# Kernel optimization log

Hardware: AMD Instinct MI355X
Metric: run time of the kernel (lower is better)

## Reference

```python
import jax, jax.numpy as jnp
import numpy as np

HIDDEN = 896
N_HEADS = 14
N_KV_HEADS = 2
HEAD_DIM = HIDDEN // N_HEADS  # 64
KV_GROUPS = N_HEADS // N_KV_HEADS  # 7
ROPE_THETA = 1000000.0


def rotate_half(x):
    x1, x2 = x[..., : x.shape[-1] // 2], x[..., x.shape[-1] // 2 :]
    return jnp.concatenate((-x2, x1), axis=-1)


def rope_tables(seq_len, dtype=jnp.float32):
    inv_freq = 1.0 / (ROPE_THETA ** (jnp.arange(0, HEAD_DIM, 2, dtype=jnp.float32) / HEAD_DIM))
    t = jnp.arange(seq_len, dtype=jnp.float32)
    freqs = jnp.outer(t, inv_freq)            # [S, D/2]
    emb = jnp.concatenate((freqs, freqs), -1)  # [S, D]
    return jnp.cos(emb).astype(dtype), jnp.sin(emb).astype(dtype)


def setup_inputs() -> dict:
    key = jax.random.key(0)
    ks = jax.random.split(key, 8)
    B, S = 2, 2048
    s = 0.02
    return {
        "hidden_states": jax.random.normal(ks[0], (B, S, HIDDEN), jnp.float32),
        "wq": jax.random.normal(ks[1], (HIDDEN, N_HEADS * HEAD_DIM), jnp.float32) * s,
        "bq": jnp.zeros((N_HEADS * HEAD_DIM,), jnp.float32),
        "wk": jax.random.normal(ks[2], (HIDDEN, N_KV_HEADS * HEAD_DIM), jnp.float32) * s,
        "bk": jnp.zeros((N_KV_HEADS * HEAD_DIM,), jnp.float32),
        "wv": jax.random.normal(ks[3], (HIDDEN, N_KV_HEADS * HEAD_DIM), jnp.float32) * s,
        "bv": jnp.zeros((N_KV_HEADS * HEAD_DIM,), jnp.float32),
        "wo": jax.random.normal(ks[4], (N_HEADS * HEAD_DIM, HIDDEN), jnp.float32) * s,
    }


def reference(hidden_states, wq, bq, wk, bk, wv, bv, wo):
    B, S, _ = hidden_states.shape
    q = (hidden_states @ wq + bq).reshape(B, S, N_HEADS, HEAD_DIM)
    k = (hidden_states @ wk + bk).reshape(B, S, N_KV_HEADS, HEAD_DIM)
    v = (hidden_states @ wv + bv).reshape(B, S, N_KV_HEADS, HEAD_DIM)

    cos, sin = rope_tables(S, hidden_states.dtype)
    cos, sin = cos[None, :, None, :], sin[None, :, None, :]
    q = q * cos + rotate_half(q) * sin
    k = k * cos + rotate_half(k) * sin

    # GQA broadcast: repeat kv heads to match query heads
    k = jnp.repeat(k, KV_GROUPS, axis=2)
    v = jnp.repeat(v, KV_GROUPS, axis=2)

    # [B, H, S, S]
    scores = jnp.einsum("bqhd,bkhd->bhqk", q, k) / jnp.sqrt(jnp.asarray(HEAD_DIM, hidden_states.dtype))
    mask = jnp.tril(jnp.ones((S, S), dtype=jnp.bool_))
    scores = jnp.where(mask[None, None, :, :], scores, jnp.asarray(-1e9, scores.dtype))
    attn = jax.nn.softmax(scores, axis=-1)
    out = jnp.einsum("bhqk,bkhd->bqhd", attn, v).reshape(B, S, N_HEADS * HEAD_DIM)
    return out @ wo
```

## Files before the change

### kernel.cpp

```cpp
#include <hip/hip_runtime.h>

#define HID 896
#define NQ 896
#define NKV 128
#define NQKV 1152
#define NH 14
#define NKVH 2
#define GQ 7
#define DH 64
#define SEQ 2048
#define BATCH 2
#define TOK (BATCH*SEQ)

typedef __attribute__((ext_vector_type(8))) short short8;
typedef __attribute__((ext_vector_type(4))) float f32x4;
typedef __attribute__((ext_vector_type(4))) unsigned short us4;

__device__ __forceinline__ unsigned short f2bf(float x) {
  unsigned int u = __builtin_bit_cast(unsigned int, x);
  u = (u + 0x7fffu + ((u >> 16) & 1u)) >> 16;
  return (unsigned short)u;
}
__device__ __forceinline__ float bf2f(unsigned short b) {
  return __builtin_bit_cast(float, (unsigned int)b << 16);
}
__device__ __forceinline__ f32x4 fzero4() {
  f32x4 z; z[0]=0.f; z[1]=0.f; z[2]=0.f; z[3]=0.f; return z;
}
__device__ __forceinline__ unsigned int cvt_pk_bf16(float lo, float hi) {
  unsigned int r;
  asm("v_cvt_pk_bf16_f32 %0, %1, %2" : "=v"(r) : "v"(lo), "v"(hi));
  return r;
}
__device__ __forceinline__ void gload_lds16(const unsigned short* g, unsigned short* l) {
  __builtin_amdgcn_global_load_lds(
      (const __attribute__((address_space(1))) void*)(const void*)g,
      (__attribute__((address_space(3))) void*)(void*)l, 16, 0, 0);
}

#define CVT_BLKS 3584
#define TRN_BLKS 448
#define BIAS_BLKS 5
#define TAB_BLKS 256
#define PREP_BLKS (CVT_BLKS + TRN_BLKS + BIAS_BLKS + TAB_BLKS)

__global__ void k_prep(const float* __restrict__ hs,
                       const float* __restrict__ wq, const float* __restrict__ bq,
                       const float* __restrict__ wk, const float* __restrict__ bk,
                       const float* __restrict__ wv, const float* __restrict__ bv,
                       const float* __restrict__ wo,
                       unsigned short* __restrict__ hb,
                       unsigned short* __restrict__ wqkvt,
                       unsigned short* __restrict__ wot,
                       float* __restrict__ bqkv,
                       float* __restrict__ ct, float* __restrict__ st) {
  __shared__ unsigned short Ls[64*65];
  int blk = blockIdx.x, tid = threadIdx.x;
  if (blk < CVT_BLKS) {
    int i = blk*256 + tid;
    float4 v = ((const float4*)hs)[i];
    us4 o; o[0]=f2bf(v.x); o[1]=f2bf(v.y); o[2]=f2bf(v.z); o[3]=f2bf(v.w);
    ((us4*)hb)[i] = o;
    return;
  }
  blk -= CVT_BLKS;
  if (blk < TRN_BLKS) {
    const float* W; unsigned short* out; int K, N, n0, k0;
    if (blk < 196)      { W=wq; out=wqkvt;                        K=HID; N=NQ;  int t=blk;     n0=(t%14)*64; k0=(t/14)*64; }
    else if (blk < 224) { W=wk; out=wqkvt + (size_t)NQ*HID;       K=HID; N=NKV; int t=blk-196; n0=(t%2)*64;  k0=(t/2)*64; }
    else if (blk < 252) { W=wv; out=wqkvt + (size_t)(NQ+NKV)*HID; K=HID; N=NKV; int t=blk-224; n0=(t%2)*64;  k0=(t/2)*64; }
    else                { W=wo; out=wot;                          K=NQ;  N=HID; int t=blk-252; n0=(t%14)*64; k0=(t/14)*64; }
    #pragma unroll
    for (int i = 0; i < 16; ++i) {
      int idx = i*256 + tid;
      int r = idx >> 6, c = idx & 63;
      Ls[c*65 + r] = f2bf(W[(size_t)(k0 + r)*N + n0 + c]);
    }
    __syncthreads();
    #pragma unroll
    for (int i = 0; i < 16; ++i) {
      int idx = i*256 + tid;
      int r2 = idx >> 6, c2 = idx & 63;
      out[(size_t)(n0 + r2)*K + k0 + c2] = Ls[r2*65 + c2];
    }
    return;
  }
  blk -= TRN_BLKS;
  if (blk < BIAS_BLKS) {
    int i = blk*256 + tid;
    if (i < NQKV) {
      if (i < NQ) bqkv[i] = bq[i];
      else if (i < NQ + NKV) bqkv[i] = bk[i - NQ];
      else bqkv[i] = bv[i - NQ - NKV];
    }
    return;
  }
  blk -= BIAS_BLKS;
  {
    int i = blk*256 + tid;
    int s = i >> 5, dp = i & 31;
    float inv = __expf(-(float)(2*dp) * (13.815510557964274f / 64.0f));
    float f = (float)s * inv;
    ct[i] = cosf(f); st[i] = sinf(f);
  }
}

template<int OUTMODE>
__global__ __launch_bounds__(256, 2) void k_gemm_bt(
    const unsigned short* __restrict__ A,
    const unsigned short* __restrict__ Bt,
    const float* __restrict__ bias,
    void* __restrict__ Cout,
    int M, int N, int K) {
  __shared__ unsigned short As[128*64];
  __shared__ unsigned short Bs[128*64];
  int tid = threadIdx.x;
  int lane = tid & 63, w = tid >> 6;
  int wr = w >> 1, wc = w & 1;
  int l15 = lane & 15, l4 = lane >> 4;
  int m0 = blockIdx.y * 128, n0 = blockIdx.x * 128;

  f32x4 acc[4][4];
  #pragma unroll
  for (int i = 0; i < 4; ++i)
    #pragma unroll
    for (int j = 0; j < 4; ++j) acc[i][j] = fzero4();

  int nkt = K >> 6;
  for (int kt = 0; kt < nkt; ++kt) {
    int k0 = kt << 6;
    #pragma unroll
    for (int t = 0; t < 4; ++t) {
      int chunk = t*256 + w*64 + lane;
      int row = chunk >> 3, sp = chunk & 7;
      int sl = sp ^ (row & 7);
      gload_lds16(A + (size_t)(m0+row)*K + k0 + sl*8, &As[(t*256 + w*64)*8]);
      gload_lds16(Bt + (size_t)(n0+row)*K + k0 + sl*8, &Bs[(t*256 + w*64)*8]);
    }
    __syncthreads();
    #pragma unroll
    for (int s = 0; s < 2; ++s) {
      short8 af[4], bfr[4];
      #pragma unroll
      for (int mi = 0; mi < 4; ++mi) {
        int row = wr*64 + mi*16 + l15;
        int slot = (s*4 + l4) ^ (row & 7);
        af[mi] = *reinterpret_cast<const short8*>(&As[row*64 + slot*8]);
      }
      #pragma unroll
      for (int ni = 0; ni < 4; ++ni) {
        int row = wc*64 + ni*16 + l15;
        int slot = (s*4 + l4) ^ (row & 7);
        bfr[ni] = *reinterpret_cast<const short8*>(&Bs[row*64 + slot*8]);
      }
      #pragma unroll
      for (int mi = 0; mi < 4; ++mi)
        #pragma unroll
        for (int ni = 0; ni < 4; ++ni)
          acc[mi][ni] = __builtin_amdgcn_mfma_f32_16x16x32_bf16(af[mi], bfr[ni], acc[mi][ni], 0, 0, 0);
    }
    __syncthreads();
  }
  #pragma unroll
  for (int mi = 0; mi < 4; ++mi) {
    #pragma unroll
    for (int ni = 0; ni < 4; ++ni) {
      #pragma unroll
      for (int r = 0; r < 4; ++r) {
        int row = m0 + wr*64 + mi*16 + l4*4 + r;
        int col = n0 + wc*64 + ni*16 + l15;
        float v = acc[mi][ni][r];
        if (OUTMODE == 0) {
          v += bias[col];
          ((unsigned short*)Cout)[(size_t)row*N + col] = f2bf(v);
        } else {
          ((float*)Cout)[(size_t)row*N + col] = v;
        }
      }
    }
  }
}

__global__ void k_rope(const unsigned short* __restrict__ qkv,
                       const float* __restrict__ ct, const float* __restrict__ st,
                       unsigned short* __restrict__ Qr, unsigned short* __restrict__ Kr,
                       unsigned short* __restrict__ Vt) {
  int t = blockIdx.x; int b = t >> 11; int s = t & 2047;
  int tid = threadIdx.x;
  const unsigned short* row = qkv + (size_t)t * NQKV;
  if (tid < 448) {
    int h = tid >> 5, dp = tid & 31;
    float x1 = bf2f(row[h*64 + dp]);
    float x2 = bf2f(row[h*64 + dp + 32]);
    float c = ct[s*32 + dp], sn = st[s*32 + dp];
    size_t base = (((size_t)b*NH + h)*SEQ + s)*64;
    Qr[base + dp]      = f2bf((x1*c - x2*sn) * 0.125f);
    Qr[base + dp + 32] = f2bf((x2*c + x1*sn) * 0.125f);
  } else {
    int j = tid - 448;
    int kvh = j >> 5, dp = j & 31;
    float x1 = bf2f(row[NQ + kvh*64 + dp]);
    float x2 = bf2f(row[NQ + kvh*64 + dp + 32]);
    float c = ct[s*32 + dp], sn = st[s*32 + dp];
    size_t base = (((size_t)b*NKVH + kvh)*SEQ + s)*64;
    Kr[base + dp]      = f2bf(x1*c - x2*sn);
    Kr[base + dp + 32] = f2bf(x2*c + x1*sn);
  }
  if (tid < 128) {
    int kvh = tid >> 6, d = tid & 63;
    Vt[(((size_t)b*NKVH + kvh)*64 + d)*SEQ + s] = row[1024 + kvh*64 + d];
  }
}

__global__ __launch_bounds__(256, 2) void k_attn(
    const unsigned short* __restrict__ Q,
    const unsigned short* __restrict__ Kr,
    const unsigned short* __restrict__ Vt,
    unsigned short* __restrict__ Aout) {
  __shared__ __align__(16) unsigned short Kst[2][64*64];
  __shared__ __align__(16) unsigned short Vst[2][64*64];
  __shared__ __align__(16) unsigned short P_lds[2][4*16*64];
  int lane = threadIdx.x & 63, w = threadIdx.x >> 6;
  int l15 = lane & 15, l4 = lane >> 4;
  int i = blockIdx.x, h = blockIdx.y, b = blockIdx.z;
  int qtH = 31 - i, qtL = i;
  int kvh = h / GQ;
  const unsigned short* Kb = Kr + ((size_t)(b*NKVH + kvh))*SEQ*64;
  const unsigned short* Vb = Vt + ((size_t)(b*NKVH + kvh))*64*SEQ;
  char* PwH = (char*)&P_lds[0][w*16*64];
  char* PwL = (char*)&P_lds[1][w*16*64];

  auto stage = [&](int kt, int bsel) {
    #pragma unroll
    for (int t = 0; t < 2; ++t) {
      int chunk = t*256 + w*64 + lane;
      int row = chunk >> 3;
      int sl = (chunk & 7) ^ (row & 7);
      gload_lds16(Kb + (size_t)(kt*64 + row)*64 + sl*8, &Kst[bsel][(t*256 + w*64)*8]);
      gload_lds16(Vb + (size_t)row*SEQ + kt*64 + sl*8, &Vst[bsel][(t*256 + w*64)*8]);
    }
  };

  const unsigned short* QbH = Q + (((size_t)(b*NH + h))*SEQ + qtH*64 + w*16) * 64;
  const unsigned short* QbL = Q + (((size_t)(b*NH + h))*SEQ + qtL*64 + w*16) * 64;
  short8 qaH[2], qaL[2];
  #pragma unroll
  for (int s = 0; s < 2; ++s) {
    qaH[s] = *reinterpret_cast<const short8*>(QbH + l15*64 + s*32 + l4*8);
    qaL[s] = *reinterpret_cast<const short8*>(QbL + l15*64 + s*32 + l4*8);
  }

  f32x4 accH[4], accL[4];
  #pragma unroll
  for (int n = 0; n < 4; ++n) { accH[n] = fzero4(); accL[n] = fzero4(); }
  float mH = -__builtin_inff(), lH = 0.0f;
  float mL = -__builtin_inff(), lL = 0.0f;

  int cur = 0;

  auto tile = [&](int kt, bool diag, short8 (&qa)[2], f32x4 (&acc)[4],
                  float& m_run, float& l_run, int qt, char* Pwb) {
    f32x4 sa[4];
    #pragma unroll
    for (int n = 0; n < 4; ++n) sa[n] = fzero4();
    #pragma unroll
    for (int s = 0; s < 2; ++s) {
      short8 kb[4];
      #pragma unroll
      for (int n = 0; n < 4; ++n) {
        int row = n*16 + l15;
        int slot = (s*4 + l4) ^ (row & 7);
        kb[n] = *reinterpret_cast<const short8*>(&Kst[cur][row*64 + slot*8]);
      }
      #pragma unroll
      for (int n = 0; n < 4; ++n)
        sa[n] = __builtin_amdgcn_mfma_f32_16x16x32_bf16(kb[n], qa[s], sa[n], 0, 0, 0);
    }
    if (diag) {
      int q_glob = qt*64 + w*16 + l15;
      #pragma unroll
      for (int n = 0; n < 4; ++n)
        #pragma unroll
        for (int r = 0; r < 4; ++r) {
          int kpos = kt*64 + n*16 + l4*4 + r;
          if (kpos > q_glob) sa[n][r] = -1e30f;
        }
    }
    float t01 = fmaxf(fmaxf(sa[0][0],sa[0][1]), fmaxf(sa[0][2],sa[0][3]));
    float t11 = fmaxf(fmaxf(sa[1][0],sa[1][1]), fmaxf(sa[1][2],sa[1][3]));
    float t21 = fmaxf(fmaxf(sa[2][0],sa[2][1]), fmaxf(sa[2][2],sa[2][3]));
    float t31 = fmaxf(fmaxf(sa[3][0],sa[3][1]), fmaxf(sa[3][2],sa[3][3]));
    float tmax = fmaxf(fmaxf(t01,t11), fmaxf(t21,t31));
    tmax = fmaxf(tmax, __shfl_xor(tmax, 16));
    tmax = fmaxf(tmax, __shfl_xor(tmax, 32));
    float mn = fmaxf(m_run, tmax);
    float sc = __expf(m_run - mn);
    #pragma unroll
    for (int n = 0; n < 4; ++n)
      #pragma unroll
      for (int r = 0; r < 4; ++r) sa[n][r] = __expf(sa[n][r] - mn);
    float s0 = (sa[0][0]+sa[0][1]) + (sa[0][2]+sa[0][3]);
    float s1 = (sa[1][0]+sa[1][1]) + (sa[1][2]+sa[1][3]);
    float s2r = (sa[2][0]+sa[2][1]) + (sa[2][2]+sa[2][3]);
    float s3 = (sa[3][0]+sa[3][1]) + (sa[3][2]+sa[3][3]);
    float sum = (s0+s1) + (s2r+s3);
    sum += __shfl_xor(sum, 16);
    sum += __shfl_xor(sum, 32);
    m_run = mn;
    l_run = l_run*sc + sum;
    #pragma unroll
    for (int n = 0; n < 4; ++n) acc[n] *= sc;
    #pragma unroll
    for (int n = 0; n < 4; ++n) {
      uint2 pk;
      pk.x = cvt_pk_bf16(sa[n][0], sa[n][1]);
      pk.y = cvt_pk_bf16(sa[n][2], sa[n][3]);
      int colbyte = n*32 + l4*8;
      int addr = l15*128 + ((((colbyte>>4) ^ (l15&7))) << 4) + (colbyte & 15);
      *reinterpret_cast<uint2*>(Pwb + addr) = pk;
    }
    #pragma unroll
    for (int s2 = 0; s2 < 2; ++s2) {
      int pslot = (s2*4 + l4) ^ (l15 & 7);
      short8 pa = *reinterpret_cast<const short8*>(Pwb + l15*128 + pslot*16);
      #pragma unroll
      for (int n = 0; n < 4; ++n) {
        int row = n*16 + l15;
        int vslot = (s2*4 + l4) ^ (row & 7);
        short8 vb = *reinterpret_cast<const short8*>(&Vst[cur][row*64 + vslot*8]);
        acc[n] = __builtin_amdgcn_mfma_f32_16x16x32_bf16(vb, pa, acc[n], 0, 0, 0);
      }
    }
  };

  stage(0, 0);
  __syncthreads();
  int nkt = qtH + 1;
  for (int kt = 0; kt < nkt; ++kt) {
    if (kt + 1 < nkt) stage(kt + 1, cur ^ 1);
    tile(kt, kt == qtH, qaH, accH, mH, lH, qtH, PwH);
    if (kt <= qtL) tile(kt, kt == qtL, qaL, accL, mL, lL, qtL, PwL);
    __syncthreads();
    cur ^= 1;
  }

  auto epi = [&](f32x4 (&acc)[4], float l_run, int qt, char* Pwb) {
    float inv = 1.0f / l_run;
    #pragma unroll
    for (int n = 0; n < 4; ++n) {
      uint2 pk;
      pk.x = cvt_pk_bf16(acc[n][0]*inv, acc[n][1]*inv);
      pk.y = cvt_pk_bf16(acc[n][2]*inv, acc[n][3]*inv);
      int colbyte = n*32 + l4*8;
      int addr = l15*128 + ((((colbyte>>4) ^ (l15&7))) << 4) + (colbyte & 15);
      *reinterpret_cast<uint2*>(Pwb + addr) = pk;
    }
    int row = lane >> 2;
    int cb0 = (lane & 3) * 32;
    #pragma unroll
    for (int it = 0; it < 2; ++it) {
      int cb = cb0 + it*16;
      int slot = (cb >> 4) ^ (row & 7);
      short8 v = *reinterpret_cast<const short8*>(Pwb + row*128 + slot*16);
      size_t tok = (size_t)b*SEQ + qt*64 + w*16 + row;
      *reinterpret_cast<short8*>(&Aout[tok*NQ + h*64 + (cb>>1)]) = v;
    }
  };
  epi(accH, lH, qtH, PwH);
  epi(accL, lL, qtL, PwL);
}

extern "C" void kernel_launch(void* const* d_in, const int* in_sizes, int n_in,
                              void* d_out, int out_size, void* d_ws, size_t ws_size,
                              hipStream_t stream) {
  const float* hs = (const float*)d_in[0];
  const float* wq = (const float*)d_in[1];
  const float* bq = (const float*)d_in[2];
  const float* wk = (const float*)d_in[3];
  const float* bk = (const float*)d_in[4];
  const float* wv = (const float*)d_in[5];
  const float* bv = (const float*)d_in[6];
  const float* wo = (const float*)d_in[7];
  float* out = (float*)d_out;

  char* p = (char*)d_ws;
  auto alloc = [&](size_t bytes) { char* r = p; p += (bytes + 255) & ~(size_t)255; return r; };
  unsigned short* hb    = (unsigned short*)alloc((size_t)TOK*HID*2);
  unsigned short* wqkvt = (unsigned short*)alloc((size_t)NQKV*HID*2);
  unsigned short* wot   = (unsigned short*)alloc((size_t)HID*NQ*2);
  float*          bqkv  = (float*)alloc(NQKV*4);
  unsigned short* qkvt  = (unsigned short*)alloc((size_t)TOK*NQKV*2);
  unsigned short* q_r   = (unsigned short*)alloc((size_t)BATCH*NH*SEQ*DH*2);
  unsigned short* k_r   = (unsigned short*)alloc((size_t)BATCH*NKVH*SEQ*DH*2);
  unsigned short* v_t   = (unsigned short*)alloc((size_t)BATCH*NKVH*DH*SEQ*2);
  float*          ct    = (float*)alloc((size_t)SEQ*32*4);
  float*          st    = (float*)alloc((size_t)SEQ*32*4);
  unsigned short* attn  = hb;

  k_prep<<<PREP_BLKS, 256, 0, stream>>>(hs, wq, bq, wk, bk, wv, bv, wo,
                                        hb, wqkvt, wot, bqkv, ct, st);
  k_gemm_bt<0><<<dim3(NQKV/128, TOK/128), 256, 0, stream>>>(hb, wqkvt, bqkv, qkvt, TOK, NQKV, HID);
  k_rope<<<TOK, 512, 0, stream>>>(qkvt, ct, st, q_r, k_r, v_t);
  k_attn<<<dim3(16, NH, BATCH), 256, 0, stream>>>(q_r, k_r, v_t, attn);
  k_gemm_bt<1><<<dim3(NQ/128, TOK/128), 256, 0, stream>>>(attn, wot, nullptr, out, TOK, NQ, HID);
}
```

Before: 104.1 us.

## Drop LDS K/V staging in attention, load directly from global, one q-tile per block

The attention kernel no longer stages K and V tiles into double-buffered shared memory with barriers. Each wave now reads its K and V fragments straight from global memory (relying on cache), and the paired high/low q-tile scheme is replaced by one q-tile per block with a doubled grid. Occupancy is raised to 3 blocks per CU because shared memory use shrinks to the P buffer. This removes the per-tile __syncthreads and LDS staging cost, but every wave now issues its own K/V global loads with no cross-wave reuse, and causal load balancing now depends on reversed block ordering.

Result: slower. 285.6 us (+174.4%).

```diff
diff --git a/kernel.cpp b/kernel.cpp
--- a/kernel.cpp
+++ b/kernel.cpp
@@ -212,54 +212,33 @@
   }
 }
 
-__global__ __launch_bounds__(256, 2) void k_attn(
+__global__ __launch_bounds__(256, 3) void k_attn(
     const unsigned short* __restrict__ Q,
     const unsigned short* __restrict__ Kr,
     const unsigned short* __restrict__ Vt,
     unsigned short* __restrict__ Aout) {
-  __shared__ __align__(16) unsigned short Kst[2][64*64];
-  __shared__ __align__(16) unsigned short Vst[2][64*64];
-  __shared__ __align__(16) unsigned short P_lds[2][4*16*64];
+  __shared__ __align__(16) unsigned short P_lds[4][16*64];
   int lane = threadIdx.x & 63, w = threadIdx.x >> 6;
   int l15 = lane & 15, l4 = lane >> 4;
-  int i = blockIdx.x, h = blockIdx.y, b = blockIdx.z;
-  int qtH = 31 - i, qtL = i;
+  int qt = (int)gridDim.x - 1 - (int)blockIdx.x;
+  int h = blockIdx.y, b = blockIdx.z;
   int kvh = h / GQ;
   const unsigned short* Kb = Kr + ((size_t)(b*NKVH + kvh))*SEQ*64;
   const unsigned short* Vb = Vt + ((size_t)(b*NKVH + kvh))*64*SEQ;
-  char* PwH = (char*)&P_lds[0][w*16*64];
-  char* PwL = (char*)&P_lds[1][w*16*64];
-
-  auto stage = [&](int kt, int bsel) {
-    #pragma unroll
-    for (int t = 0; t < 2; ++t) {
-      int chunk = t*256 + w*64 + lane;
-      int row = chunk >> 3;
-      int sl = (chunk & 7) ^ (row & 7);
-      gload_lds16(Kb + (size_t)(kt*64 + row)*64 + sl*8, &Kst[bsel][(t*256 + w*64)*8]);
-      gload_lds16(Vb + (size_t)row*SEQ + kt*64 + sl*8, &Vst[bsel][(t*256 + w*64)*8]);
-    }
-  };
-
-  const unsigned short* QbH = Q + (((size_t)(b*NH + h))*SEQ + qtH*64 + w*16) * 64;
-  const unsigned short* QbL = Q + (((size_t)(b*NH + h))*SEQ + qtL*64 + w*16) * 64;
-  short8 qaH[2], qaL[2];
-  #pragma unroll
-  for (int s = 0; s < 2; ++s) {
-    qaH[s] = *reinterpret_cast<const short8*>(QbH + l15*64 + s*32 + l4*8);
-    qaL[s] = *reinterpret_cast<const short8*>(QbL + l15*64 + s*32 + l4*8);
-  }
-
-  f32x4 accH[4], accL[4];
-  #pragma unroll
-  for (int n = 0; n < 4; ++n) { accH[n] = fzero4(); accL[n] = fzero4(); }
-  float mH = -__builtin_inff(), lH = 0.0f;
-  float mL = -__builtin_inff(), lL = 0.0f;
-
-  int cur = 0;
-
-  auto tile = [&](int kt, bool diag, short8 (&qa)[2], f32x4 (&acc)[4],
-                  float& m_run, float& l_run, int qt, char* Pwb) {
+  char* Pw = (char*)&P_lds[w][0];
+
+  const unsigned short* Qb = Q + (((size_t)(b*NH + h))*SEQ + qt*64 + w*16) * 64;
+  short8 qa[2];
+  #pragma unroll
+  for (int s = 0; s < 2; ++s)
+    qa[s] = *reinterpret_cast<const short8*>(Qb + l15*64 + s*32 + l4*8);
+
+  f32x4 acc[4];
+  #pragma unroll
+  for (int n = 0; n < 4; ++n) acc[n] = fzero4();
+  float m_run = -__builtin_inff(), l_run = 0.0f;
+
+  for (int kt = 0; kt <= qt; ++kt) {
     f32x4 sa[4];
     #pragma unroll
     for (int n = 0; n < 4; ++n) sa[n] = fzero4();
@@ -267,16 +246,21 @@
     for (int s = 0; s < 2; ++s) {
       short8 kb[4];
       #pragma unroll
-      for (int n = 0; n < 4; ++n) {
-        int row = n*16 + l15;
-        int slot = (s*4 + l4) ^ (row & 7);
-        kb[n] = *reinterpret_cast<const short8*>(&Kst[cur][row*64 + slot*8]);
-      }
+      for (int n = 0; n < 4; ++n)
+        kb[n] = *reinterpret_cast<const short8*>(
+            Kb + (size_t)(kt*64 + n*16 + l15)*64 + s*32 + l4*8);
       #pragma unroll
       for (int n = 0; n < 4; ++n)
         sa[n] = __builtin_amdgcn_mfma_f32_16x16x32_bf16(kb[n], qa[s], sa[n], 0, 0, 0);
     }
-    if (diag) {
+    short8 vb[2][4];
+    #pragma unroll
+    for (int s2 = 0; s2 < 2; ++s2)
+      #pragma unroll
+      for (int n = 0; n < 4; ++n)
+        vb[s2][n] = *reinterpret_cast<const short8*>(
+            Vb + (size_t)(n*16 + l15)*SEQ + kt*64 + s2*32 + l4*8);
+    if (kt == qt) {
       int q_glob = qt*64 + w*16 + l15;
       #pragma unroll
       for (int n = 0; n < 4; ++n)
@@ -286,11 +270,11 @@
           if (kpos > q_glob) sa[n][r] = -1e30f;
         }
     }
-    float t01 = fmaxf(fmaxf(sa[0][0],sa[0][1]), fmaxf(sa[0][2],sa[0][3]));
-    float t11 = fmaxf(fmaxf(sa[1][0],sa[1][1]), fmaxf(sa[1][2],sa[1][3]));
-    float t21 = fmaxf(fmaxf(sa[2][0],sa[2][1]), fmaxf(sa[2][2],sa[2][3]));
-    float t31 = fmaxf(fmaxf(sa[3][0],sa[3][1]), fmaxf(sa[3][2],sa[3][3]));
-    float tmax = fmaxf(fmaxf(t01,t11), fmaxf(t21,t31));
+    float t0 = fmaxf(fmaxf(sa[0][0],sa[0][1]), fmaxf(sa[0][2],sa[0][3]));
+    float t1 = fmaxf(fmaxf(sa[1][0],sa[1][1]), fmaxf(sa[1][2],sa[1][3]));
+    float t2 = fmaxf(fmaxf(sa[2][0],sa[2][1]), fmaxf(sa[2][2],sa[2][3]));
+    float t3 = fmaxf(fmaxf(sa[3][0],sa[3][1]), fmaxf(sa[3][2],sa[3][3]));
+    float tmax = fmaxf(fmaxf(t0,t1), fmaxf(t2,t3));
     tmax = fmaxf(tmax, __shfl_xor(tmax, 16));
     tmax = fmaxf(tmax, __shfl_xor(tmax, 32));
     float mn = fmaxf(m_run, tmax);
@@ -301,9 +285,9 @@
       for (int r = 0; r < 4; ++r) sa[n][r] = __expf(sa[n][r] - mn);
     float s0 = (sa[0][0]+sa[0][1]) + (sa[0][2]+sa[0][3]);
     float s1 = (sa[1][0]+sa[1][1]) + (sa[1][2]+sa[1][3]);
-    float s2r = (sa[2][0]+sa[2][1]) + (sa[2][2]+sa[2][3]);
+    float s2 = (sa[2][0]+sa[2][1]) + (sa[2][2]+sa[2][3]);
     float s3 = (sa[3][0]+sa[3][1]) + (sa[3][2]+sa[3][3]);
-    float sum = (s0+s1) + (s2r+s3);
+    float sum = (s0+s1) + (s2+s3);
     sum += __shfl_xor(sum, 16);
     sum += __shfl_xor(sum, 32);
     m_run = mn;
@@ -317,57 +301,38 @@
       pk.y = cvt_pk_bf16(sa[n][2], sa[n][3]);
       int colbyte = n*32 + l4*8;
       int addr = l15*128 + ((((colbyte>>4) ^ (l15&7))) << 4) + (colbyte & 15);
-      *reinterpret_cast<uint2*>(Pwb + addr) = pk;
-    }
-    #pragma unroll
-    for (int s2 = 0; s2 < 2; ++s2) {
-      int pslot = (s2*4 + l4) ^ (l15 & 7);
-      short8 pa = *reinterpret_cast<const short8*>(Pwb + l15*128 + pslot*16);
-      #pragma unroll
-      for (int n = 0; n < 4; ++n) {
-        int row = n*16 + l15;
-        int vslot = (s2*4 + l4) ^ (row & 7);
-        short8 vb = *reinterpret_cast<const short8*>(&Vst[cur][row*64 + vslot*8]);
-        acc[n] = __builtin_amdgcn_mfma_f32_16x16x32_bf16(vb, pa, acc[n], 0, 0, 0);
-      }
-    }
-  };
-
-  stage(0, 0);
-  __syncthreads();
-  int nkt = qtH + 1;
-  for (int kt = 0; kt < nkt; ++kt) {
-    if (kt + 1 < nkt) stage(kt + 1, cur ^ 1);
-    tile(kt, kt == qtH, qaH, accH, mH, lH, qtH, PwH);
-    if (kt <= qtL) tile(kt, kt == qtL, qaL, accL, mL, lL, qtL, PwL);
-    __syncthreads();
-    cur ^= 1;
-  }
-
-  auto epi = [&](f32x4 (&acc)[4], float l_run, int qt, char* Pwb) {
-    float inv = 1.0f / l_run;
-    #pragma unroll
-    for (int n = 0; n < 4; ++n) {
-      uint2 pk;
-      pk.x = cvt_pk_bf16(acc[n][0]*inv, acc[n][1]*inv);
-      pk.y = cvt_pk_bf16(acc[n][2]*inv, acc[n][3]*inv);
-      int colbyte = n*32 + l4*8;
-      int addr = l15*128 + ((((colbyte>>4) ^ (l15&7))) << 4) + (colbyte & 15);
-      *reinterpret_cast<uint2*>(Pwb + addr) = pk;
-    }
-    int row = lane >> 2;
-    int cb0 = (lane & 3) * 32;
-    #pragma unroll
-    for (int it = 0; it < 2; ++it) {
-      int cb = cb0 + it*16;
-      int slot = (cb >> 4) ^ (row & 7);
-      short8 v = *reinterpret_cast<const short8*>(Pwb + row*128 + slot*16);
-      size_t tok = (size_t)b*SEQ + qt*64 + w*16 + row;
-      *reinterpret_cast<short8*>(&Aout[tok*NQ + h*64 + (cb>>1)]) = v;
-    }
-  };
-  epi(accH, lH, qtH, PwH);
-  epi(accL, lL, qtL, PwL);
+      *reinterpret_cast<uint2*>(Pw + addr) = pk;
+    }
+    #pragma unroll
+    for (int s2i = 0; s2i < 2; ++s2i) {
+      int pslot = (s2i*4 + l4) ^ (l15 & 7);
+      short8 pa = *reinterpret_cast<const short8*>(Pw + l15*128 + pslot*16);
+      #pragma unroll
+      for (int n = 0; n < 4; ++n)
+        acc[n] = __builtin_amdgcn_mfma_f32_16x16x32_bf16(vb[s2i][n], pa, acc[n], 0, 0, 0);
+    }
+  }
+
+  float inv = 1.0f / l_run;
+  #pragma unroll
+  for (int n = 0; n < 4; ++n) {
+    uint2 pk;
+    pk.x = cvt_pk_bf16(acc[n][0]*inv, acc[n][1]*inv);
+    pk.y = cvt_pk_bf16(acc[n][2]*inv, acc[n][3]*inv);
+    int colbyte = n*32 + l4*8;
+    int addr = l15*128 + ((((colbyte>>4) ^ (l15&7))) << 4) + (colbyte & 15);
+    *reinterpret_cast<uint2*>(Pw + addr) = pk;
+  }
+  int row = lane >> 2;
+  int cb0 = (lane & 3) * 32;
+  #pragma unroll
+  for (int it = 0; it < 2; ++it) {
+    int cb = cb0 + it*16;
+    int slot = (cb >> 4) ^ (row & 7);
+    short8 v = *reinterpret_cast<const short8*>(Pw + row*128 + slot*16);
+    size_t tok = (size_t)b*SEQ + qt*64 + w*16 + row;
+    *reinterpret_cast<short8*>(&Aout[tok*NQ + h*64 + (cb>>1)]) = v;
+  }
 }
 
 extern "C" void kernel_launch(void* const* d_in, const int* in_sizes, int n_in,
@@ -401,6 +366,6 @@
                                         hb, wqkvt, wot, bqkv, ct, st);
   k_gemm_bt<0><<<dim3(NQKV/128, TOK/128), 256, 0, stream>>>(hb, wqkvt, bqkv, qkvt, TOK, NQKV, HID);
   k_rope<<<TOK, 512, 0, stream>>>(qkvt, ct, st, q_r, k_r, v_t);
-  k_attn<<<dim3(16, NH, BATCH), 256, 0, stream>>>(q_r, k_r, v_t, attn);
+  k_attn<<<dim3(32, NH, BATCH), 256, 0, stream>>>(q_r, k_r, v_t, attn);
   k_gemm_bt<1><<<dim3(NQ/128, TOK/128), 256, 0, stream>>>(attn, wot, nullptr, out, TOK, NQ, HID);
 }
```
